# Kernel optimization log

Measured on AMD Instinct MI355X. Metric: run time of the kernel, lower is better.

## Reference

```python
import jax, jax.numpy as jnp
import numpy as np

B, N, E = 8, 10000, 160000
D_IN, D_H = 128, 128
EPS = 1e-5


def setup_inputs() -> dict:
    key = jax.random.key(0)
    ks = jax.random.split(key, 10)
    x = jax.random.normal(ks[0], (B, N, D_IN), dtype=jnp.float32)
    h_prev = jax.random.normal(ks[1], (B, N, D_H), dtype=jnp.float32)
    edge_index = jax.random.randint(ks[2], (2, E), 0, N, dtype=jnp.int32)
    d_cat = D_IN + D_H
    s = 1.0 / np.sqrt(d_cat)
    def w(k):
        return jax.random.uniform(k, (d_cat, D_H), jnp.float32, -s, s)
    def b(k):
        return jax.random.uniform(k, (D_H,), jnp.float32, -s, s)
    return {
        "x": x, "edge_index": edge_index, "h_prev": h_prev,
        "Wz": w(ks[3]), "bz": b(ks[4]),
        "Wr": w(ks[5]), "br": b(ks[6]),
        "Wc": w(ks[7]), "bc": b(ks[8]),
        "gamma": jnp.ones((D_H,), jnp.float32),
        "beta": jnp.zeros((D_H,), jnp.float32),
    }


def _gcn(x, W, bias, src, dst, norm, n_nodes):
    # PyG GCNConv: linear transform, gather from src, weight by sym-norm, scatter-add to dst
    msg = (x @ W)[src] * norm[:, None]          # [E_total, D_H]
    return jax.ops.segment_sum(msg, dst, num_segments=n_nodes) + bias


def reference(x, edge_index, h_prev, Wz, bz, Wr, br, Wc, bc, gamma, beta):
    Bx, Nx, _ = x.shape
    BN = Bx * Nx
    x_flat = x.reshape(BN, -1)
    h_flat = h_prev.reshape(BN, -1)

    # batch the edge index with per-graph node offsets (all edges are in-range)
    offsets = (jnp.arange(Bx, dtype=edge_index.dtype) * Nx)[:, None]
    src = (edge_index[0][None, :] + offsets).reshape(-1)
    dst = (edge_index[1][None, :] + offsets).reshape(-1)

    # GCN self-loops + symmetric normalization (shared by all three convs)
    loops = jnp.arange(BN, dtype=src.dtype)
    src = jnp.concatenate([src, loops])
    dst = jnp.concatenate([dst, loops])
    deg = jax.ops.segment_sum(jnp.ones_like(dst, dtype=x.dtype), dst, num_segments=BN)
    dis = jnp.where(deg > 0, 1.0 / jnp.sqrt(jnp.maximum(deg, 1.0)), 0.0)
    norm = dis[src] * dis[dst]

    xh = jnp.concatenate([x_flat, h_flat], axis=1)
    z = jax.nn.sigmoid(_gcn(xh, Wz, bz, src, dst, norm, BN))
    r = jax.nn.sigmoid(_gcn(xh, Wr, br, src, dst, norm, BN))
    xrh = jnp.concatenate([x_flat, r * h_flat], axis=1)
    h_cand = jnp.tanh(_gcn(xrh, Wc, bc, src, dst, norm, BN))

    h_new = (1.0 - z) * h_flat + z * h_cand

    # LayerNorm over last dim
    mu = h_new.mean(axis=-1, keepdims=True)
    var = ((h_new - mu) ** 2).mean(axis=-1, keepdims=True)
    h_new = (h_new - mu) / jnp.sqrt(var + EPS) * gamma + beta
    return h_new.reshape(Bx, Nx, -1)
```

## Files before the change

### kernel.cpp

```cpp
#include <hip/hip_runtime.h>

#define NN 10000
#define BB 8
#define EE 160000
#define DH 128
#define LN_EPS 1e-5f

typedef unsigned short ushort_t;
typedef unsigned int uint_t;

typedef __bf16 bf16x8 __attribute__((ext_vector_type(8)));
typedef float floatx4 __attribute__((ext_vector_type(4)));
typedef float floatx2 __attribute__((ext_vector_type(2)));

__device__ __forceinline__ float b2f(uint_t u) { return __uint_as_float(u << 16); }
__device__ __forceinline__ ushort_t f2b(float f) {
    uint_t u = __float_as_uint(f);
    return (ushort_t)((u + 0x7fffu + ((u >> 16) & 1u)) >> 16);
}
__device__ __forceinline__ uint_t pack2(float lo, float hi) {
    return (uint_t)f2b(lo) | ((uint_t)f2b(hi) << 16);
}
__device__ __forceinline__ float sigm(float x) { return 1.0f / (1.0f + __expf(-x)); }
__device__ __forceinline__ float tanh_fast(float x) {
    float ex = __expf(2.0f * x);
    return 1.0f - 2.0f / (ex + 1.0f);
}

__device__ __forceinline__ floatx2 unpk(uint_t u) {
    floatx2 r;
    r.x = __uint_as_float(u << 16);
    r.y = __uint_as_float(u & 0xffff0000u);
    return r;
}
__device__ __forceinline__ void pk_fma(floatx2& a, floatx2 w, floatx2 v) {
    asm("v_pk_fma_f32 %0, %1, %2, %0" : "+v"(a) : "v"(w), "v"(v));
}
__device__ __forceinline__ void acc8p(floatx2* a, floatx2 w2, uint4 v) {
    pk_fma(a[0], w2, unpk(v.x));
    pk_fma(a[1], w2, unpk(v.y));
    pk_fma(a[2], w2, unpk(v.z));
    pk_fma(a[3], w2, unpk(v.w));
}


__global__ __launch_bounds__(256) void scan1(const int* __restrict__ cnt,
                                             int* __restrict__ offs,
                                             int* __restrict__ bsum) {
    __shared__ int s[256];
    const int t = threadIdx.x, idx = blockIdx.x * 256 + t;
    int x = (idx < NN) ? cnt[idx] : 0;
    s[t] = x;
    __syncthreads();
    for (int o = 1; o < 256; o <<= 1) {
        int v = s[t];
        int u = (t >= o) ? s[t - o] : 0;
        __syncthreads();
        s[t] = v + u;
        __syncthreads();
    }
    if (idx < NN) offs[idx] = s[t] - x;
    if (t == 255) bsum[blockIdx.x] = s[255];
}

__global__ __launch_bounds__(256) void scan3(const int* __restrict__ cnt,
                                             const int* __restrict__ bsum,
                                             int* __restrict__ offs,
                                             int* __restrict__ cursor,
                                             float* __restrict__ dis) {
    __shared__ int sb[40];
    __shared__ int pfx;
    const int t = threadIdx.x;
    if (t < 40) sb[t] = bsum[t];
    __syncthreads();
    if (t == 0) {
        int a = 0;
        for (int i = 0; i < blockIdx.x; ++i) a += sb[i];
        pfx = a;
    }
    __syncthreads();
    const int idx = blockIdx.x * 256 + t;
    if (idx < NN) {
        int off = offs[idx] + pfx;
        offs[idx] = off;
        cursor[idx] = off;
        dis[idx] = rsqrtf((float)(cnt[idx] + 1));
    }
    if (idx == 0) offs[NN] = EE;
}

__global__ void fill_csr(const int* __restrict__ ei, int* __restrict__ cursor,
                         const float* __restrict__ dis, int* __restrict__ csr_pk) {
    int e = blockIdx.x * 256 + threadIdx.x;
    if (e < EE) {
        int s = ei[e];
        int d = ei[EE + e];
        int pos = atomicAdd(&cursor[d], 1);
        csr_pk[pos] = (int)(((uint_t)f2b(dis[s]) << 16) | (uint_t)s);
    }
}


__global__ __launch_bounds__(256) void cp_k(const int* __restrict__ ei,
                                            int* __restrict__ cnt,
                                            const float* __restrict__ x,
                                            const float* __restrict__ h,
                                            ushort_t* __restrict__ xhb,
                                            const float* __restrict__ Wz,
                                            const float* __restrict__ Wr,
                                            const float* __restrict__ Wc,
                                            ushort_t* __restrict__ Wt_zr,
                                            ushort_t* __restrict__ Wt_c) {
    if (blockIdx.x < 625) {
        int e = blockIdx.x * 256 + threadIdx.x;
        atomicAdd(&cnt[ei[EE + e]], 1);
        return;
    }
    const int bid = blockIdx.x - 625;
    if (bid < 10000) {
        const size_t o = ((size_t)bid * 256 + threadIdx.x) * 4;
        const size_t row = o >> 7, col = o & 127;
        float4 vx = *(const float4*)(x + o);
        uint2 px;
        px.x = pack2(vx.x, vx.y);
        px.y = pack2(vx.z, vx.w);
        *(uint2*)(xhb + row * 256 + col) = px;
        float4 vh = *(const float4*)(h + o);
        uint2 ph;
        ph.x = pack2(vh.x, vh.y);
        ph.y = pack2(vh.z, vh.w);
        *(uint2*)(xhb + row * 256 + 128 + col) = ph;
    } else {
        const int col = bid - 10000, k = threadIdx.x;
        if (col < 256) {
            float v = (col < 128) ? Wz[(size_t)k * 128 + col]
                                  : Wr[(size_t)k * 128 + col - 128];
            Wt_zr[(size_t)col * 256 + k] = f2b(v);
        } else {
            int c2 = col - 256;
            Wt_c[(size_t)c2 * 256 + k] = f2b(Wc[(size_t)k * 128 + c2]);
        }
    }
}


template <int MODE>
__global__ __launch_bounds__(256) void gather16(
    const ushort_t* __restrict__ src, const int* __restrict__ offs,
    const int* __restrict__ csr_pk, const float* __restrict__ dis,
    ushort_t* __restrict__ dst) {
    const int tid = threadIdx.x, lane = tid & 63;
    const int b = blockIdx.x & 7;
    const int g = lane >> 4, il = lane & 15;
    const int ng = (blockIdx.x >> 3) * 16 + (tid >> 6) * 4 + g;
    const uint_t SST = (MODE == 0) ? 256u : 128u;
    const ushort_t* base = src + (size_t)b * NN * SST;
    const uint_t cofs = (uint_t)il * 8u;

    floatx2 a0[4], a1[4];
#pragma unroll
    for (int j = 0; j < 4; ++j) {
        a0[j] = (floatx2){0.f, 0.f};
        a1[j] = (floatx2){0.f, 0.f};
    }

    const int e0 = offs[ng], e1 = offs[ng + 1];
    const float dn = dis[ng];

    {
        const floatx2 d2 = {dn, dn};
        const uint_t off = (uint_t)ng * SST + cofs;
        acc8p(a0, d2, *(const uint4*)(base + off));
        if (MODE == 0) acc8p(a1, d2, *(const uint4*)(base + off + 128));
    }

    int mx = e1 - e0;
    mx = max(mx, __shfl_xor(mx, 16));
    mx = max(mx, __shfl_xor(mx, 32));
    const int dmax = __builtin_amdgcn_readfirstlane(mx);
    const int pbase = (lane & 48) << 2;

    for (int ibase = 0; ibase < dmax; ibase += 16) {
        int pk = 0;
        const int pos = e0 + ibase + il;
        if (pos < e1) pk = csr_pk[pos];
        const int lim = (dmax - ibase) < 16 ? (dmax - ibase) : 16;

#define PROC8(OFF)                                                                   \
    {                                                                                \
        int p[8];                                                                    \
        uint_t q[8];                                                                 \
        _Pragma("unroll") for (int k = 0; k < 8; ++k) p[k] =                         \
            __builtin_amdgcn_ds_bpermute(pbase + ((OFF) + k) * 4, pk);               \
        _Pragma("unroll") for (int k = 0; k < 8; ++k) q[k] =                         \
            (uint_t)(p[k] & 0xffff) * SST + cofs;                                    \
        uint4 v[8];                                                                  \
        _Pragma("unroll") for (int k = 0; k < 8; ++k) v[k] =                         \
            *(const uint4*)(base + q[k]);                                            \
        uint4 u[8];                                                                  \
        if (MODE == 0) {                                                             \
            _Pragma("unroll") for (int k = 0; k < 8; ++k) u[k] =                     \
                *(const uint4*)(base + q[k] + 128);                                  \
        }                                                                            \
        _Pragma("unroll") for (int k = 0; k < 8; ++k) {                              \
            const float f = __uint_as_float((uint_t)p[k] & 0xffff0000u);             \
            const floatx2 w2 = {f, f};                                               \
            acc8p(a0, w2, v[k]);                                                     \
            if (MODE == 0) acc8p(a1, w2, u[k]);                                      \
        }                                                                            \
    }
        PROC8(0);
        if (lim > 8) PROC8(8);
#undef PROC8
    }

    const size_t o = ((size_t)b * NN + ng) * 256 + cofs;
    uint4 st;
    st.x = pack2(a0[0].x * dn, a0[0].y * dn);
    st.y = pack2(a0[1].x * dn, a0[1].y * dn);
    st.z = pack2(a0[2].x * dn, a0[2].y * dn);
    st.w = pack2(a0[3].x * dn, a0[3].y * dn);
    if (MODE == 0) {
        *(uint4*)(dst + o) = st;
        uint4 st1;
        st1.x = pack2(a1[0].x * dn, a1[0].y * dn);
        st1.y = pack2(a1[1].x * dn, a1[1].y * dn);
        st1.z = pack2(a1[2].x * dn, a1[2].y * dn);
        st1.w = pack2(a1[3].x * dn, a1[3].y * dn);
        *(uint4*)(dst + o + 128) = st1;
    } else {
        *(uint4*)(dst + o + 128) = st;
    }
}


__global__ __launch_bounds__(512) void gemm_zr(
    const ushort_t* __restrict__ A, const ushort_t* __restrict__ Wt,
    const float* __restrict__ bz, const float* __restrict__ br,
    const float* __restrict__ h_prev, ushort_t* __restrict__ z_out,
    ushort_t* __restrict__ rh_out) {
    __shared__ __align__(16) ushort_t As[128 * 72];
    __shared__ __align__(16) ushort_t Bs[256 * 72];
    const int tid = threadIdx.x;
    const int rb0 = blockIdx.x * 128;
    const int wv = tid >> 6, lane = tid & 63;
    const int l15 = lane & 15, qq = lane >> 4;
    const int sr = tid >> 2;
    const int kh = (tid & 3) * 16;
    const int sc = tid >> 1;
    const int kb = (tid & 1) * 32;

    floatx4 acc[16];
#pragma unroll
    for (int j = 0; j < 16; ++j) acc[j] = (floatx4){0.f, 0.f, 0.f, 0.f};

    uint4 pa0, pa1, pb0, pb1, pb2, pb3;
#define LOAD_AB(k0)                                                     \
    {                                                                   \
        const ushort_t* sA = A + (size_t)(rb0 + sr) * 256 + (k0) + kh;  \
        pa0 = *(const uint4*)(sA);                                      \
        pa1 = *(const uint4*)(sA + 8);                                  \
        const ushort_t* sB = Wt + (size_t)sc * 256 + (k0) + kb;         \
        pb0 = *(const uint4*)(sB);                                      \
        pb1 = *(const uint4*)(sB + 8);                                  \
        pb2 = *(const uint4*)(sB + 16);                                 \
        pb3 = *(const uint4*)(sB + 24);                                 \
    }

    LOAD_AB(0);
#pragma unroll
    for (int t = 0; t < 4; ++t) {
        if (t) __syncthreads();
        *(uint4*)(&As[sr * 72 + kh]) = pa0;
        *(uint4*)(&As[sr * 72 + kh + 8]) = pa1;
        *(uint4*)(&Bs[sc * 72 + kb]) = pb0;
        *(uint4*)(&Bs[sc * 72 + kb + 8]) = pb1;
        *(uint4*)(&Bs[sc * 72 + kb + 16]) = pb2;
        *(uint4*)(&Bs[sc * 72 + kb + 24]) = pb3;
        __syncthreads();
        if (t < 3) LOAD_AB((t + 1) * 64);
#pragma unroll
        for (int ks = 0; ks < 2; ++ks) {
            const int ko = ks * 32 + qq * 8;
            bf16x8 a0 = *(const bf16x8*)&As[(wv * 16 + l15) * 72 + ko];
#pragma unroll
            for (int j = 0; j < 16; ++j) {
                bf16x8 b = *(const bf16x8*)&Bs[(j * 16 + l15) * 72 + ko];
                acc[j] = __builtin_amdgcn_mfma_f32_16x16x32_bf16(a0, b, acc[j], 0, 0, 0);
            }
        }
    }
#undef LOAD_AB

    float bvz[8], bvr[8];
#pragma unroll
    for (int j = 0; j < 8; ++j) {
        bvz[j] = bz[j * 16 + l15];
        bvr[j] = br[j * 16 + l15];
    }
#pragma unroll
    for (int j = 0; j < 8; ++j)
#pragma unroll
        for (int v = 0; v < 4; ++v) {
            int row = rb0 + wv * 16 + qq * 4 + v;
            z_out[(size_t)row * 128 + j * 16 + l15] = f2b(sigm(acc[j][v] + bvz[j]));
        }
#pragma unroll
    for (int j = 0; j < 8; ++j)
#pragma unroll
        for (int v = 0; v < 4; ++v) {
            int row = rb0 + wv * 16 + qq * 4 + v;
            int col = j * 16 + l15;
            float r = sigm(acc[j + 8][v] + bvr[j]);
            float hh = h_prev[(size_t)row * 128 + col];
            rh_out[(size_t)row * 128 + col] = f2b(r * hh);
        }
}


__global__ __launch_bounds__(512) void gemm_c(
    const ushort_t* __restrict__ A, const ushort_t* __restrict__ Wt,
    const float* __restrict__ bc, const float* __restrict__ h_prev,
    const ushort_t* __restrict__ z_in, const float* __restrict__ gamma,
    const float* __restrict__ beta, float* __restrict__ f_out) {
    __shared__ __align__(16) ushort_t As[128 * 72];
    __shared__ __align__(16) ushort_t Bs[128 * 72];
    const int tid = threadIdx.x;
    const int rb0 = blockIdx.x * 128;
    const int wv = tid >> 6, lane = tid & 63;
    const int l15 = lane & 15, qq = lane >> 4;
    const int sr = tid >> 2;
    const int kh = (tid & 3) * 16;

    floatx4 acc[8];
#pragma unroll
    for (int j = 0; j < 8; ++j) acc[j] = (floatx4){0.f, 0.f, 0.f, 0.f};

    uint4 pa0, pa1, pb0, pb1;
#define LOAD_AB(k0)                                                     \
    {                                                                   \
        const ushort_t* sA = A + (size_t)(rb0 + sr) * 256 + (k0) + kh;  \
        pa0 = *(const uint4*)(sA);                                      \
        pa1 = *(const uint4*)(sA + 8);                                  \
        const ushort_t* sB = Wt + (size_t)sr * 256 + (k0) + kh;         \
        pb0 = *(const uint4*)(sB);                                      \
        pb1 = *(const uint4*)(sB + 8);                                  \
    }

    LOAD_AB(0);
#pragma unroll
    for (int t = 0; t < 4; ++t) {
        if (t) __syncthreads();
        *(uint4*)(&As[sr * 72 + kh]) = pa0;
        *(uint4*)(&As[sr * 72 + kh + 8]) = pa1;
        *(uint4*)(&Bs[sr * 72 + kh]) = pb0;
        *(uint4*)(&Bs[sr * 72 + kh + 8]) = pb1;
        __syncthreads();
        if (t < 3) LOAD_AB((t + 1) * 64);
#pragma unroll
        for (int ks = 0; ks < 2; ++ks) {
            const int ko = ks * 32 + qq * 8;
            bf16x8 a0 = *(const bf16x8*)&As[(wv * 16 + l15) * 72 + ko];
#pragma unroll
            for (int j = 0; j < 8; ++j) {
                bf16x8 b = *(const bf16x8*)&Bs[(j * 16 + l15) * 72 + ko];
                acc[j] = __builtin_amdgcn_mfma_f32_16x16x32_bf16(a0, b, acc[j], 0, 0, 0);
            }
        }
    }
#undef LOAD_AB

    float bv[8], gv[8], bev[8];
#pragma unroll
    for (int j = 0; j < 8; ++j) {
        bv[j] = bc[j * 16 + l15];
        gv[j] = gamma[j * 16 + l15];
        bev[j] = beta[j * 16 + l15];
    }
#pragma unroll
    for (int v = 0; v < 4; ++v) {
        const int row = rb0 + wv * 16 + qq * 4 + v;
        float hn[8];
        float s = 0.f;
#pragma unroll
        for (int j = 0; j < 8; ++j) {
            float hc = tanh_fast(acc[j][v] + bv[j]);
            float zz = b2f((uint_t)z_in[(size_t)row * 128 + j * 16 + l15]);
            float hh = h_prev[(size_t)row * 128 + j * 16 + l15];
            hn[j] = (1.0f - zz) * hh + zz * hc;
            s += hn[j];
        }
#pragma unroll
        for (int o = 8; o > 0; o >>= 1) s += __shfl_xor(s, o);
        float mu = s * (1.0f / 128.0f);
        float vv = 0.f;
#pragma unroll
        for (int j = 0; j < 8; ++j) {
            float d = hn[j] - mu;
            vv += d * d;
        }
#pragma unroll
        for (int o = 8; o > 0; o >>= 1) vv += __shfl_xor(vv, o);
        float inv = rsqrtf(vv * (1.0f / 128.0f) + LN_EPS);
#pragma unroll
        for (int j = 0; j < 8; ++j)
            f_out[(size_t)row * 128 + j * 16 + l15] =
                (hn[j] - mu) * inv * gv[j] + bev[j];
    }
}


extern "C" void kernel_launch(void* const* d_in, const int* in_sizes, int n_in,
                              void* d_out, int out_size, void* d_ws, size_t ws_size,
                              hipStream_t stream) {
    const float* x = (const float*)d_in[0];
    const int* ei = (const int*)d_in[1];
    const float* h = (const float*)d_in[2];
    const float* Wz = (const float*)d_in[3];
    const float* bz = (const float*)d_in[4];
    const float* Wr = (const float*)d_in[5];
    const float* br = (const float*)d_in[6];
    const float* Wc = (const float*)d_in[7];
    const float* bcv = (const float*)d_in[8];
    const float* gamma = (const float*)d_in[9];
    const float* beta = (const float*)d_in[10];
    float* out = (float*)d_out;

    char* w = (char*)d_ws;
    int* offs = (int*)(w + 0);
    float* dis = (float*)(w + 40960);
    int* csr_pk = (int*)(w + 81920);
    int* cnt = (int*)(w + 721920);
    int* cursor = (int*)(w + 762880);
    int* bsum = (int*)(w + 803840);
    ushort_t* Wt_zr = (ushort_t*)(w + 1041920);
    ushort_t* Wt_c = (ushort_t*)(w + 1172992);
    ushort_t* xhb = (ushort_t*)(w + 1239040);
    ushort_t* agg_xh = (ushort_t*)(w + 42199040);
    ushort_t* z_buf = (ushort_t*)(w + 1239040);
    ushort_t* rh_bf = (ushort_t*)(w + 21719040);

    hipMemsetAsync(cnt, 0, NN * sizeof(int), stream);
    cp_k<<<11009, 256, 0, stream>>>(ei, cnt, x, h, xhb, Wz, Wr, Wc, Wt_zr, Wt_c);
    scan1<<<40, 256, 0, stream>>>(cnt, offs, bsum);
    scan3<<<40, 256, 0, stream>>>(cnt, bsum, offs, cursor, dis);
    fill_csr<<<EE / 256, 256, 0, stream>>>(ei, cursor, dis, csr_pk);

    gather16<0><<<(NN / 16) * 8, 256, 0, stream>>>(xhb, offs, csr_pk, dis, agg_xh);
    gemm_zr<<<80000 / 128, 512, 0, stream>>>(agg_xh, Wt_zr, bz, br, h, z_buf, rh_bf);
    gather16<1><<<(NN / 16) * 8, 256, 0, stream>>>(rh_bf, offs, csr_pk, dis, agg_xh);
    gemm_c<<<80000 / 128, 512, 0, stream>>>(agg_xh, Wt_c, bcv, h, z_buf, gamma, beta,
                                            out);
}
```

Measured before the change: 298.4 us.

## Split z/r GEMM into two column blocks via 2D grid

The fused z/r GEMM used to compute all 256 output columns in one block. It now launches a second grid dimension, so each block computes 128 columns: either the z gate or the r gate. This doubles the number of blocks (625 to 1250) and halves the accumulator registers and B-tile shared memory, which should improve occupancy and load balance across CUs. The cost is that each A tile is loaded from global memory twice, once per gate.

Result: faster. 287.3 us (-3.7%).

```diff
diff --git a/kernel.cpp b/kernel.cpp
--- a/kernel.cpp
+++ b/kernel.cpp
@@ -240,31 +240,29 @@
     const float* __restrict__ h_prev, ushort_t* __restrict__ z_out,
     ushort_t* __restrict__ rh_out) {
     __shared__ __align__(16) ushort_t As[128 * 72];
-    __shared__ __align__(16) ushort_t Bs[256 * 72];
+    __shared__ __align__(16) ushort_t Bs[128 * 72];
     const int tid = threadIdx.x;
     const int rb0 = blockIdx.x * 128;
+    const int mode = blockIdx.y;
+    const int cb0 = mode * 128;
     const int wv = tid >> 6, lane = tid & 63;
     const int l15 = lane & 15, qq = lane >> 4;
     const int sr = tid >> 2;
     const int kh = (tid & 3) * 16;
-    const int sc = tid >> 1;
-    const int kb = (tid & 1) * 32;
-
-    floatx4 acc[16];
-#pragma unroll
-    for (int j = 0; j < 16; ++j) acc[j] = (floatx4){0.f, 0.f, 0.f, 0.f};
-
-    uint4 pa0, pa1, pb0, pb1, pb2, pb3;
-#define LOAD_AB(k0)                                                     \
-    {                                                                   \
-        const ushort_t* sA = A + (size_t)(rb0 + sr) * 256 + (k0) + kh;  \
-        pa0 = *(const uint4*)(sA);                                      \
-        pa1 = *(const uint4*)(sA + 8);                                  \
-        const ushort_t* sB = Wt + (size_t)sc * 256 + (k0) + kb;         \
-        pb0 = *(const uint4*)(sB);                                      \
-        pb1 = *(const uint4*)(sB + 8);                                  \
-        pb2 = *(const uint4*)(sB + 16);                                 \
-        pb3 = *(const uint4*)(sB + 24);                                 \
+
+    floatx4 acc[8];
+#pragma unroll
+    for (int j = 0; j < 8; ++j) acc[j] = (floatx4){0.f, 0.f, 0.f, 0.f};
+
+    uint4 pa0, pa1, pb0, pb1;
+#define LOAD_AB(k0)                                                           \
+    {                                                                         \
+        const ushort_t* sA = A + (size_t)(rb0 + sr) * 256 + (k0) + kh;        \
+        pa0 = *(const uint4*)(sA);                                            \
+        pa1 = *(const uint4*)(sA + 8);                                        \
+        const ushort_t* sB = Wt + (size_t)(cb0 + sr) * 256 + (k0) + kh;       \
+        pb0 = *(const uint4*)(sB);                                            \
+        pb1 = *(const uint4*)(sB + 8);                                        \
     }
 
     LOAD_AB(0);
@@ -273,10 +271,8 @@
         if (t) __syncthreads();
         *(uint4*)(&As[sr * 72 + kh]) = pa0;
         *(uint4*)(&As[sr * 72 + kh + 8]) = pa1;
-        *(uint4*)(&Bs[sc * 72 + kb]) = pb0;
-        *(uint4*)(&Bs[sc * 72 + kb + 8]) = pb1;
-        *(uint4*)(&Bs[sc * 72 + kb + 16]) = pb2;
-        *(uint4*)(&Bs[sc * 72 + kb + 24]) = pb3;
+        *(uint4*)(&Bs[sr * 72 + kh]) = pb0;
+        *(uint4*)(&Bs[sr * 72 + kh + 8]) = pb1;
         __syncthreads();
         if (t < 3) LOAD_AB((t + 1) * 64);
 #pragma unroll
@@ -284,7 +280,7 @@
             const int ko = ks * 32 + qq * 8;
             bf16x8 a0 = *(const bf16x8*)&As[(wv * 16 + l15) * 72 + ko];
 #pragma unroll
-            for (int j = 0; j < 16; ++j) {
+            for (int j = 0; j < 8; ++j) {
                 bf16x8 b = *(const bf16x8*)&Bs[(j * 16 + l15) * 72 + ko];
                 acc[j] = __builtin_amdgcn_mfma_f32_16x16x32_bf16(a0, b, acc[j], 0, 0, 0);
             }
@@ -292,29 +288,31 @@
     }
 #undef LOAD_AB
 
-    float bvz[8], bvr[8];
-#pragma unroll
-    for (int j = 0; j < 8; ++j) {
-        bvz[j] = bz[j * 16 + l15];
-        bvr[j] = br[j * 16 + l15];
-    }
-#pragma unroll
-    for (int j = 0; j < 8; ++j)
-#pragma unroll
-        for (int v = 0; v < 4; ++v) {
-            int row = rb0 + wv * 16 + qq * 4 + v;
-            z_out[(size_t)row * 128 + j * 16 + l15] = f2b(sigm(acc[j][v] + bvz[j]));
-        }
-#pragma unroll
-    for (int j = 0; j < 8; ++j)
-#pragma unroll
-        for (int v = 0; v < 4; ++v) {
-            int row = rb0 + wv * 16 + qq * 4 + v;
-            int col = j * 16 + l15;
-            float r = sigm(acc[j + 8][v] + bvr[j]);
-            float hh = h_prev[(size_t)row * 128 + col];
-            rh_out[(size_t)row * 128 + col] = f2b(r * hh);
-        }
+    if (mode == 0) {
+        float bv[8];
+#pragma unroll
+        for (int j = 0; j < 8; ++j) bv[j] = bz[j * 16 + l15];
+#pragma unroll
+        for (int j = 0; j < 8; ++j)
+#pragma unroll
+            for (int v = 0; v < 4; ++v) {
+                int row = rb0 + wv * 16 + qq * 4 + v;
+                z_out[(size_t)row * 128 + j * 16 + l15] = f2b(sigm(acc[j][v] + bv[j]));
+            }
+    } else {
+        float bv[8];
+#pragma unroll
+        for (int j = 0; j < 8; ++j) bv[j] = br[j * 16 + l15];
+#pragma unroll
+        for (int j = 0; j < 8; ++j)
+#pragma unroll
+            for (int v = 0; v < 4; ++v) {
+                int row = rb0 + wv * 16 + qq * 4 + v;
+                float r = sigm(acc[j][v] + bv[j]);
+                float hh = h_prev[(size_t)row * 128 + j * 16 + l15];
+                rh_out[(size_t)row * 128 + j * 16 + l15] = f2b(r * hh);
+            }
+    }
 }
 
 
@@ -447,7 +445,8 @@
     fill_csr<<<EE / 256, 256, 0, stream>>>(ei, cursor, dis, csr_pk);
 
     gather16<0><<<(NN / 16) * 8, 256, 0, stream>>>(xhb, offs, csr_pk, dis, agg_xh);
-    gemm_zr<<<80000 / 128, 512, 0, stream>>>(agg_xh, Wt_zr, bz, br, h, z_buf, rh_bf);
+    gemm_zr<<<dim3(80000 / 128, 2), 512, 0, stream>>>(agg_xh, Wt_zr, bz, br, h,
+                                                      z_buf, rh_bf);
     gather16<1><<<(NN / 16) * 8, 256, 0, stream>>>(rh_bf, offs, csr_pk, dis, agg_xh);
     gemm_c<<<80000 / 128, 512, 0, stream>>>(agg_xh, Wt_c, bcv, h, z_buf, gamma, beta,
                                             out);
```
